# Optimization experiments

Measured on AMD Instinct MI355X. Metric: run time of the kernel, lower is better.

Reference implementation:

```python
import jax, jax.numpy as jnp
import numpy as np

INPUT_DIM = 512
HIDDEN_DIM = 512
B, N = 8, 2048


def setup_inputs() -> dict:
    key = jax.random.key(0)
    ks = jax.random.split(key, 9)
    s_in = 1.0 / np.sqrt(INPUT_DIM)
    s_h = 1.0 / np.sqrt(HIDDEN_DIM)
    return {
        "X": jax.random.normal(ks[0], (B, N, INPUT_DIM), dtype=jnp.float32),
        "Wq": jax.random.uniform(ks[1], (INPUT_DIM, HIDDEN_DIM), minval=-s_in, maxval=s_in),
        "bq": jnp.zeros((HIDDEN_DIM,), jnp.float32),
        "Wk": jax.random.uniform(ks[2], (INPUT_DIM, HIDDEN_DIM), minval=-s_in, maxval=s_in),
        "bk": jnp.zeros((HIDDEN_DIM,), jnp.float32),
        "Wv": jax.random.uniform(ks[3], (INPUT_DIM, HIDDEN_DIM), minval=-s_in, maxval=s_in),
        "bv": jnp.zeros((HIDDEN_DIM,), jnp.float32),
        "Wo": jax.random.uniform(ks[4], (HIDDEN_DIM, INPUT_DIM), minval=-s_h, maxval=s_h),
        "bo": jnp.zeros((INPUT_DIM,), jnp.float32),
        "ln_gamma": jnp.ones((INPUT_DIM,), jnp.float32),
        "ln_beta": jnp.zeros((INPUT_DIM,), jnp.float32),
    }


def reference(X, Wq, bq, Wk, bk, Wv, bv, Wo, bo, ln_gamma, ln_beta):
    q = X @ Wq + bq                      # [B,N,H]
    k = X @ Wk + bk
    v = X @ Wv + bv
    scores = jnp.einsum('bnh,bmh->bnm', q, k) / jnp.sqrt(jnp.float32(HIDDEN_DIM))
    attn = jax.nn.softmax(scores, axis=-1)      # [B,N,N]
    ctx = jnp.einsum('bnm,bmh->bnh', attn, v)   # [B,N,H]
    out = ctx @ Wo + bo + X                      # residual
    mu = jnp.mean(out, axis=-1, keepdims=True)
    var = jnp.var(out, axis=-1, keepdims=True)
    normed = (out - mu) / jnp.sqrt(var + 1e-5)
    return normed * ln_gamma + ln_beta
```

## Files before the change

### kernel.cpp

```cpp
#include <hip/hip_runtime.h>
#include <cstdint>
#include <cstddef>


typedef __bf16 bf16x8 __attribute__((ext_vector_type(8)));
typedef float  f32x4  __attribute__((ext_vector_type(4)));

__device__ __forceinline__ uint16_t f2bf(float f) {
  union { float f; uint32_t u; } v; v.f = f;
  uint32_t r = v.u + 0x7FFFu + ((v.u >> 16) & 1u);
  return (uint16_t)(r >> 16);
}

__device__ __forceinline__ void gld16(const uint16_t* g, uint16_t* l) {
  __builtin_amdgcn_global_load_lds(
      (__attribute__((address_space(1))) void*)(g),
      (__attribute__((address_space(3))) void*)(l), 16, 0, 0);
}

template <int MODE, int BM, int BN, int WM, int WN>
__global__ __launch_bounds__(512, 4) void gemm_k(
    const uint16_t* __restrict__ A, const uint16_t* __restrict__ Bt,
    void* __restrict__ OutA, uint16_t* __restrict__ OutK,
    uint16_t* __restrict__ OutVT, float* __restrict__ rsum, int K, int lda,
    int ldb, const float* __restrict__ b0, const float* __restrict__ b1,
    const float* __restrict__ b2, const float* __restrict__ Xres, float scale) {
  constexpr int MT = (BM / WM) / 16;
  constexpr int NT = (BN / WN) / 16;
  constexpr int AI = BM / 128;
  constexpr int BI = BN / 128;
  constexpr int PW = AI + BI;
  __shared__ alignas(16) uint16_t As[3][BM * 32];
  __shared__ alignas(16) uint16_t Bs[3][BN * 32];

  const int tid = threadIdx.x;
  const int w = tid >> 6, lane = tid & 63;
  const int wm = w / WN, wn = w % WN;

  const int gx = gridDim.x, gy = gridDim.y;
  const int nwg = gx * gy * gridDim.z;
  const int hw = blockIdx.x + gx * (blockIdx.y + gy * blockIdx.z);
  const int lg = (hw & 7) * (nwg >> 3) + (hw >> 3);
  const int bx = lg % gx, byz = lg / gx;
  const int by = byz % gy, z = byz / gy;

  const int m0 = by * BM, n0 = bx * BN;

  const uint16_t* Ab = A;
  const uint16_t* Bb = Bt;
  if (MODE == 1) { Ab += (size_t)z * 2048 * 512;  Bb += (size_t)z * 2048 * 512; }
  if (MODE == 2) { Ab += (size_t)z * 2048 * 2048; Bb += (size_t)z * 512 * 2048; }

  const int kc = (((lane & 3) ^ ((lane >> 2) & 3) ^ (lane >> 4)) * 8);
  const int rbA = w * (BM / 8);
  const int rbB = w * (BN / 8);
  const uint16_t* gA = Ab + (size_t)(m0 + rbA + (lane >> 2)) * lda + kc;
  const uint16_t* gB = Bb + (size_t)(n0 + rbB + (lane >> 2)) * ldb + kc;

  f32x4 acc[MT][NT];
#pragma unroll
  for (int i = 0; i < MT; i++)
#pragma unroll
    for (int j = 0; j < NT; j++) acc[i][j] = (f32x4){0.f, 0.f, 0.f, 0.f};

  const int lr = lane & 15;
  const int swz = (((lane >> 4) ^ (lr & 3) ^ (lr >> 2)) * 8);
  const int iters = K >> 5;

  auto stage = [&](int t, int buf) {
    const int k0 = t * 32;
#pragma unroll
    for (int j = 0; j < AI; j++)
      gld16(gA + k0 + (size_t)(j * 16) * lda, &As[buf][(rbA + j * 16) * 32]);
#pragma unroll
    for (int j = 0; j < BI; j++)
      gld16(gB + k0 + (size_t)(j * 16) * ldb, &Bs[buf][(rbB + j * 16) * 32]);
  };

  auto compute = [&](int buf) {
    bf16x8 af[MT], bfr[NT];
#pragma unroll
    for (int t = 0; t < MT; t++)
      af[t] = *(const bf16x8*)&As[buf][(wm * (BM / WM) + t * 16 + lr) * 32 + swz];
#pragma unroll
    for (int t = 0; t < NT; t++)
      bfr[t] = *(const bf16x8*)&Bs[buf][(wn * (BN / WN) + t * 16 + lr) * 32 + swz];
#pragma unroll
    for (int nt = 0; nt < NT; nt++)
#pragma unroll
      for (int mt = 0; mt < MT; mt++)
        acc[mt][nt] = __builtin_amdgcn_mfma_f32_16x16x32_bf16(
            af[mt], bfr[nt], acc[mt][nt], 0, 0, 0);
  };

  stage(0, 0);
  stage(1, 1);
  int buf = 0;
  for (int i = 0; i < iters - 1; ++i) {
    asm volatile("s_waitcnt vmcnt(%0)" ::"i"(PW) : "memory");
    __builtin_amdgcn_s_barrier();
    if (i + 2 < iters) stage(i + 2, (buf + 2 >= 3) ? buf - 1 : buf + 2);
    compute(buf);
    buf = (buf == 2) ? 0 : buf + 1;
  }
  asm volatile("s_waitcnt vmcnt(0)" ::: "memory");
  __builtin_amdgcn_s_barrier();
  compute(buf);

  if (MODE == 1) {
    uint16_t* Sp = (uint16_t*)OutA + (size_t)z * 2048 * 2048;
#pragma unroll
    for (int mt = 0; mt < MT; mt++) {
      float rp[4] = {0.f, 0.f, 0.f, 0.f};
#pragma unroll
      for (int nt = 0; nt < NT; nt++) {
#pragma unroll
        for (int i = 0; i < 4; i++) {
          const int row = m0 + wm * (BM / WM) + mt * 16 + (lane >> 4) * 4 + i;
          const int col = n0 + wn * (BN / WN) + nt * 16 + lr;
          const float e = __expf(acc[mt][nt][i] * scale);
          Sp[(size_t)row * 2048 + col] = f2bf(e);
          rp[i] += e;
        }
      }
#pragma unroll
      for (int i = 0; i < 4; i++) {
        float p = rp[i];
        p += __shfl_xor(p, 1); p += __shfl_xor(p, 2);
        p += __shfl_xor(p, 4); p += __shfl_xor(p, 8);
        if (lr == 0) {
          const int row = m0 + wm * (BM / WM) + mt * 16 + (lane >> 4) * 4 + i;
          atomicAdd(&rsum[z * 2048 + row], p);
        }
      }
    }
  } else if (MODE == 2) {
#pragma unroll
    for (int mt = 0; mt < MT; mt++) {
#pragma unroll
      for (int i = 0; i < 4; i++) {
        const int row = m0 + wm * (BM / WM) + mt * 16 + (lane >> 4) * 4 + i;
        const float sc = 1.0f / rsum[z * 2048 + row];
#pragma unroll
        for (int nt = 0; nt < NT; nt++) {
          const int col = n0 + wn * (BN / WN) + nt * 16 + lr;
          ((uint16_t*)OutA)[((size_t)z * 2048 + row) * 512 + col] =
              f2bf(acc[mt][nt][i] * sc);
        }
      }
    }
  } else {
#pragma unroll
    for (int mt = 0; mt < MT; mt++) {
#pragma unroll
      for (int nt = 0; nt < NT; nt++) {
#pragma unroll
        for (int i = 0; i < 4; i++) {
          const int row = m0 + wm * (BM / WM) + mt * 16 + (lane >> 4) * 4 + i;
          const int col = n0 + wn * (BN / WN) + nt * 16 + lr;
          const float v = acc[mt][nt][i];
          if (MODE == 0) {
            const int which = col >> 9, c = col & 511;
            if (which == 0) {
              ((uint16_t*)OutA)[(size_t)row * 512 + c] = f2bf(v + b0[c]);
            } else if (which == 1) {
              OutK[(size_t)row * 512 + c] = f2bf(v + b1[c]);
            } else {
              OutVT[(size_t)(row >> 11) * (512 * 2048) + (size_t)c * 2048 +
                    (row & 2047)] = f2bf(v + b2[c]);
            }
          } else {
            const size_t idx = (size_t)row * 512 + col;
            ((float*)OutA)[idx] = v + b0[col] + Xres[idx];
          }
        }
      }
    }
  }
}

__global__ __launch_bounds__(256) void cvt_all_k(
    const float* __restrict__ X, uint16_t* __restrict__ Xb,
    const float* __restrict__ Wq, const float* __restrict__ Wk,
    const float* __restrict__ Wv, const float* __restrict__ Wo,
    uint16_t* __restrict__ Wt, float* __restrict__ rsum) {
  const int i = blockIdx.x * 256 + threadIdx.x;
  const float4 f = ((const float4*)X)[i];
  uint32_t lo = (uint32_t)f2bf(f.x) | ((uint32_t)f2bf(f.y) << 16);
  uint32_t hi = (uint32_t)f2bf(f.z) | ((uint32_t)f2bf(f.w) << 16);
  ((uint2*)Xb)[i] = make_uint2(lo, hi);
  if (i < 16384) rsum[i] = 0.f;
  if (i < 2048 * 512) {
    const int n = i >> 9, kk = i & 511;
    const int which = n >> 9, c = n & 511;
    const float* W =
        (which == 0) ? Wq : (which == 1) ? Wk : (which == 2) ? Wv : Wo;
    Wt[i] = f2bf(W[kk * 512 + c]);
  }
}

__global__ __launch_bounds__(256) void ln_k(float* __restrict__ O,
                                            const float* __restrict__ g,
                                            const float* __restrict__ b) {
  const int tid = threadIdx.x, w = tid >> 6, lane = tid & 63;
  float* p = O + ((size_t)blockIdx.x * 4 + w) * 512;
  float4 v0 = ((const float4*)p)[lane];
  float4 v1 = ((const float4*)p)[64 + lane];
  float s  = v0.x + v0.y + v0.z + v0.w + v1.x + v1.y + v1.z + v1.w;
  float sq = v0.x * v0.x + v0.y * v0.y + v0.z * v0.z + v0.w * v0.w +
             v1.x * v1.x + v1.y * v1.y + v1.z * v1.z + v1.w * v1.w;
#pragma unroll
  for (int off = 32; off >= 1; off >>= 1) {
    s += __shfl_xor(s, off);
    sq += __shfl_xor(sq, off);
  }
  const float mean = s * (1.f / 512.f);
  const float var = sq * (1.f / 512.f) - mean * mean;
  const float rstd = rsqrtf(var + 1e-5f);
  const float4 g0 = ((const float4*)g)[lane], g1 = ((const float4*)g)[64 + lane];
  const float4 b0 = ((const float4*)b)[lane], b1 = ((const float4*)b)[64 + lane];
  v0.x = (v0.x - mean) * rstd * g0.x + b0.x;
  v0.y = (v0.y - mean) * rstd * g0.y + b0.y;
  v0.z = (v0.z - mean) * rstd * g0.z + b0.z;
  v0.w = (v0.w - mean) * rstd * g0.w + b0.w;
  v1.x = (v1.x - mean) * rstd * g1.x + b1.x;
  v1.y = (v1.y - mean) * rstd * g1.y + b1.y;
  v1.z = (v1.z - mean) * rstd * g1.z + b1.z;
  v1.w = (v1.w - mean) * rstd * g1.w + b1.w;
  ((float4*)p)[lane] = v0;
  ((float4*)p)[64 + lane] = v1;
}

extern "C" void kernel_launch(void* const* d_in, const int* in_sizes, int n_in,
                              void* d_out, int out_size, void* d_ws,
                              size_t ws_size, hipStream_t stream) {
  const float* X     = (const float*)d_in[0];
  const float* Wq    = (const float*)d_in[1];
  const float* bq    = (const float*)d_in[2];
  const float* bk    = (const float*)d_in[4];
  const float* Wk    = (const float*)d_in[3];
  const float* Wv    = (const float*)d_in[5];
  const float* bv    = (const float*)d_in[6];
  const float* Wo    = (const float*)d_in[7];
  const float* bo    = (const float*)d_in[8];
  const float* gamma = (const float*)d_in[9];
  const float* beta  = (const float*)d_in[10];
  float* out = (float*)d_out;

  char* ws = (char*)d_ws;
  uint16_t* S    = (uint16_t*)(ws);
  uint16_t* Xb   = (uint16_t*)(ws);
  uint16_t* Wt   = (uint16_t*)(ws + 67108864);
  uint16_t* q    = (uint16_t*)(ws + 69206016);
  uint16_t* kb   = (uint16_t*)(ws + 85983232);
  uint16_t* vT   = (uint16_t*)(ws + 102760448);
  float*    rsum = (float*)(ws + 119537664);
  uint16_t* ctx  = q;

  cvt_all_k<<<dim3(8192), dim3(256), 0, stream>>>(X, Xb, Wq, Wk, Wv, Wo, Wt,
                                                  rsum);
  gemm_k<0, 256, 128, 4, 2><<<dim3(12, 64, 1), dim3(512), 0, stream>>>(
      Xb, Wt, (void*)q, kb, vT, nullptr, 512, 512, 512, bq, bk, bv, nullptr,
      1.f);
  gemm_k<1, 256, 128, 4, 2><<<dim3(16, 8, 8), dim3(512), 0, stream>>>(
      q, kb, (void*)S, nullptr, nullptr, rsum, 512, 512, 512, nullptr, nullptr,
      nullptr, nullptr, 0.044194173824159216f);
  gemm_k<2, 256, 128, 4, 2><<<dim3(4, 8, 8), dim3(512), 0, stream>>>(
      S, vT, (void*)ctx, nullptr, nullptr, rsum, 2048, 2048, 2048, nullptr,
      nullptr, nullptr, nullptr, 1.f);
  gemm_k<3, 256, 128, 4, 2><<<dim3(4, 64, 1), dim3(512), 0, stream>>>(
      ctx, Wt + 1536 * 512, (void*)out, nullptr, nullptr, nullptr, 512, 512,
      512, bo, nullptr, nullptr, X, 1.f);
  ln_k<<<dim3(4096), dim3(256), 0, stream>>>(out, gamma, beta);
}
```

Before: 317.6 us.

## Restructure GEMM main loop with 64-wide K tiles and interleaved staging phases

Doubles the K tile per stage from 32 to 64 with a new XOR swizzle. Each K tile is split into two half-phases that interleave global-to-LDS staging with MFMA bursts raised via s_setprio. Occupancy hint drops to 2 blocks per SM to fit the larger LDS buffers. The goal is fewer barriers per unit of work and better overlap of loads with matrix math, at the cost of geometry fixed by static_assert and reduced occupancy.

```diff
diff --git a/kernel.cpp b/kernel.cpp
--- a/kernel.cpp
+++ b/kernel.cpp
@@ -19,19 +19,21 @@
 }
 
 template <int MODE, int BM, int BN, int WM, int WN>
-__global__ __launch_bounds__(512, 4) void gemm_k(
+__global__ __launch_bounds__(512, 2) void gemm_k(
     const uint16_t* __restrict__ A, const uint16_t* __restrict__ Bt,
     void* __restrict__ OutA, uint16_t* __restrict__ OutK,
     uint16_t* __restrict__ OutVT, float* __restrict__ rsum, int K, int lda,
     int ldb, const float* __restrict__ b0, const float* __restrict__ b1,
     const float* __restrict__ b2, const float* __restrict__ Xres, float scale) {
-  constexpr int MT = (BM / WM) / 16;
-  constexpr int NT = (BN / WN) / 16;
-  constexpr int AI = BM / 128;
-  constexpr int BI = BN / 128;
-  constexpr int PW = AI + BI;
-  __shared__ alignas(16) uint16_t As[3][BM * 32];
-  __shared__ alignas(16) uint16_t Bs[3][BN * 32];
+  constexpr int WR = BM / WM;
+  constexpr int WC = BN / WN;
+  constexpr int MT = WR / 16;
+  constexpr int NT = WC / 16;
+  constexpr int SA = BM / 64;
+  constexpr int SB = BN / 64;
+  static_assert(WR == 64 && WC == 64 && SA == 4 && SB == 2, "geometry");
+  __shared__ alignas(16) uint16_t As[3][BM * 64];
+  __shared__ alignas(16) uint16_t Bs[3][BN * 64];
 
   const int tid = threadIdx.x;
   const int w = tid >> 6, lane = tid & 63;
@@ -51,11 +53,18 @@
   if (MODE == 1) { Ab += (size_t)z * 2048 * 512;  Bb += (size_t)z * 2048 * 512; }
   if (MODE == 2) { Ab += (size_t)z * 2048 * 2048; Bb += (size_t)z * 512 * 2048; }
 
-  const int kc = (((lane & 3) ^ ((lane >> 2) & 3) ^ (lane >> 4)) * 8);
-  const int rbA = w * (BM / 8);
-  const int rbB = w * (BN / 8);
-  const uint16_t* gA = Ab + (size_t)(m0 + rbA + (lane >> 2)) * lda + kc;
-  const uint16_t* gB = Bb + (size_t)(n0 + rbB + (lane >> 2)) * ldb + kc;
+  const int l3 = lane >> 3, l7 = lane & 7;
+  const int csw = (l7 ^ l3) * 8;
+  const uint16_t* gAb = Ab + (size_t)(m0 + w * 8 + l3) * lda + csw;
+  const uint16_t* gBb = Bb + (size_t)(n0 + w * 8 + l3) * ldb + csw;
+  const int ldsw = w * 512;
+
+  auto stageA = [&](int v, int bufb, int kg) {
+    gld16(gAb + (size_t)(v * 64) * lda + kg, &As[bufb][v * 4096 + ldsw]);
+  };
+  auto stageB = [&](int v, int bufb, int kg) {
+    gld16(gBb + (size_t)(v * 64) * ldb + kg, &Bs[bufb][v * 4096 + ldsw]);
+  };
 
   f32x4 acc[MT][NT];
 #pragma unroll
@@ -63,49 +72,65 @@
 #pragma unroll
     for (int j = 0; j < NT; j++) acc[i][j] = (f32x4){0.f, 0.f, 0.f, 0.f};
 
-  const int lr = lane & 15;
-  const int swz = (((lane >> 4) ^ (lr & 3) ^ (lr >> 2)) * 8);
-  const int iters = K >> 5;
-
-  auto stage = [&](int t, int buf) {
-    const int k0 = t * 32;
-#pragma unroll
-    for (int j = 0; j < AI; j++)
-      gld16(gA + k0 + (size_t)(j * 16) * lda, &As[buf][(rbA + j * 16) * 32]);
-#pragma unroll
-    for (int j = 0; j < BI; j++)
-      gld16(gB + k0 + (size_t)(j * 16) * ldb, &Bs[buf][(rbB + j * 16) * 32]);
-  };
-
-  auto compute = [&](int buf) {
-    bf16x8 af[MT], bfr[NT];
-#pragma unroll
-    for (int t = 0; t < MT; t++)
-      af[t] = *(const bf16x8*)&As[buf][(wm * (BM / WM) + t * 16 + lr) * 32 + swz];
-#pragma unroll
-    for (int t = 0; t < NT; t++)
-      bfr[t] = *(const bf16x8*)&Bs[buf][(wn * (BN / WN) + t * 16 + lr) * 32 + swz];
-#pragma unroll
-    for (int nt = 0; nt < NT; nt++)
-#pragma unroll
-      for (int mt = 0; mt < MT; mt++)
-        acc[mt][nt] = __builtin_amdgcn_mfma_f32_16x16x32_bf16(
-            af[mt], bfr[nt], acc[mt][nt], 0, 0, 0);
-  };
-
-  stage(0, 0);
-  stage(1, 1);
-  int buf = 0;
-  for (int i = 0; i < iters - 1; ++i) {
-    asm volatile("s_waitcnt vmcnt(%0)" ::"i"(PW) : "memory");
-    __builtin_amdgcn_s_barrier();
-    if (i + 2 < iters) stage(i + 2, (buf + 2 >= 3) ? buf - 1 : buf + 2);
-    compute(buf);
-    buf = (buf == 2) ? 0 : buf + 1;
-  }
-  asm volatile("s_waitcnt vmcnt(0)" ::: "memory");
+  const int lr = lane & 15, q4 = lane >> 4;
+  const int rc0 = ((q4) ^ l7) * 8;
+  const int rc1 = ((4 + q4) ^ l7) * 8;
+
+  const int NK = K >> 6;
+
+#pragma unroll
+  for (int u = 0; u < SA; u++) stageA(u, 0, 0);
+#pragma unroll
+  for (int u = 0; u < SB; u++) stageB(u, 0, 0);
+#pragma unroll
+  for (int u = 0; u < SA; u++) stageA(u, 1, 64);
+#pragma unroll
+  for (int u = 0; u < SB; u++) stageB(u, 1, 64);
+  asm volatile("s_waitcnt vmcnt(6)" ::: "memory");
   __builtin_amdgcn_s_barrier();
-  compute(buf);
+
+#define QPHASE(QM, S0, S1, S2, DRAIN)                                          \
+  {                                                                            \
+    bf16x8 af0[2], af1[2], bv0[4], bv1[4];                                     \
+    _Pragma("unroll") for (int t = 0; t < 2; t++) {                            \
+      const int ra = (wm * 64 + (QM) * 32 + t * 16 + lr) * 64;                 \
+      af0[t] = *(const bf16x8*)&As[cb][ra + rc0];                              \
+      af1[t] = *(const bf16x8*)&As[cb][ra + rc1];                              \
+    }                                                                          \
+    _Pragma("unroll") for (int t = 0; t < 4; t++) {                            \
+      const int rb = (wn * 64 + t * 16 + lr) * 64;                             \
+      bv0[t] = *(const bf16x8*)&Bs[cb][rb + rc0];                              \
+      bv1[t] = *(const bf16x8*)&Bs[cb][rb + rc1];                              \
+    }                                                                          \
+    if (st) { S0; S1; S2; }                                                    \
+    __builtin_amdgcn_s_barrier();                                              \
+    __builtin_amdgcn_s_setprio(1);                                             \
+    _Pragma("unroll") for (int nt = 0; nt < 4; nt++)                           \
+      _Pragma("unroll") for (int mt = 0; mt < 2; mt++)                         \
+        acc[(QM) * 2 + mt][nt] = __builtin_amdgcn_mfma_f32_16x16x32_bf16(      \
+            af0[mt], bv0[nt], acc[(QM) * 2 + mt][nt], 0, 0, 0);                \
+    _Pragma("unroll") for (int nt = 0; nt < 4; nt++)                           \
+      _Pragma("unroll") for (int mt = 0; mt < 2; mt++)                         \
+        acc[(QM) * 2 + mt][nt] = __builtin_amdgcn_mfma_f32_16x16x32_bf16(      \
+            af1[mt], bv1[nt], acc[(QM) * 2 + mt][nt], 0, 0, 0);                \
+    __builtin_amdgcn_s_setprio(0);                                             \
+    DRAIN;                                                                     \
+    __builtin_amdgcn_s_barrier();                                              \
+  }
+
+  for (int kt = 0; kt < NK; ++kt) {
+    const int cb = kt % 3;
+    const int sbuf = (kt + 2) % 3;
+    const bool st = (kt + 2) < NK;
+    const int kg = (kt + 2) << 6;
+    QPHASE(0, stageA(0, sbuf, kg), stageA(1, sbuf, kg), stageA(2, sbuf, kg), )
+    QPHASE(1, stageA(3, sbuf, kg), stageB(0, sbuf, kg), stageB(1, sbuf, kg),
+           if (kt + 1 < NK) {
+             if (st) { asm volatile("s_waitcnt vmcnt(6)" ::: "memory"); }
+             else    { asm volatile("s_waitcnt vmcnt(0)" ::: "memory"); }
+           })
+  }
+#undef QPHASE
 
   if (MODE == 1) {
     uint16_t* Sp = (uint16_t*)OutA + (size_t)z * 2048 * 2048;
@@ -116,8 +141,8 @@
       for (int nt = 0; nt < NT; nt++) {
 #pragma unroll
         for (int i = 0; i < 4; i++) {
-          const int row = m0 + wm * (BM / WM) + mt * 16 + (lane >> 4) * 4 + i;
-          const int col = n0 + wn * (BN / WN) + nt * 16 + lr;
+          const int row = m0 + wm * WR + mt * 16 + (lane >> 4) * 4 + i;
+          const int col = n0 + wn * WC + nt * 16 + lr;
           const float e = __expf(acc[mt][nt][i] * scale);
           Sp[(size_t)row * 2048 + col] = f2bf(e);
           rp[i] += e;
@@ -129,7 +154,7 @@
         p += __shfl_xor(p, 1); p += __shfl_xor(p, 2);
         p += __shfl_xor(p, 4); p += __shfl_xor(p, 8);
         if (lr == 0) {
-          const int row = m0 + wm * (BM / WM) + mt * 16 + (lane >> 4) * 4 + i;
+          const int row = m0 + wm * WR + mt * 16 + (lane >> 4) * 4 + i;
           atomicAdd(&rsum[z * 2048 + row], p);
         }
       }
@@ -139,11 +164,11 @@
     for (int mt = 0; mt < MT; mt++) {
 #pragma unroll
       for (int i = 0; i < 4; i++) {
-        const int row = m0 + wm * (BM / WM) + mt * 16 + (lane >> 4) * 4 + i;
+        const int row = m0 + wm * WR + mt * 16 + (lane >> 4) * 4 + i;
         const float sc = 1.0f / rsum[z * 2048 + row];
 #pragma unroll
         for (int nt = 0; nt < NT; nt++) {
-          const int col = n0 + wn * (BN / WN) + nt * 16 + lr;
+          const int col = n0 + wn * WC + nt * 16 + lr;
           ((uint16_t*)OutA)[((size_t)z * 2048 + row) * 512 + col] =
               f2bf(acc[mt][nt][i] * sc);
         }
@@ -156,8 +181,8 @@
       for (int nt = 0; nt < NT; nt++) {
 #pragma unroll
         for (int i = 0; i < 4; i++) {
-          const int row = m0 + wm * (BM / WM) + mt * 16 + (lane >> 4) * 4 + i;
-          const int col = n0 + wn * (BN / WN) + nt * 16 + lr;
+          const int row = m0 + wm * WR + mt * 16 + (lane >> 4) * 4 + i;
+          const int col = n0 + wn * WC + nt * 16 + lr;
           const float v = acc[mt][nt][i];
           if (MODE == 0) {
             const int which = col >> 9, c = col & 511;
@@ -237,8 +262,8 @@
   const float* X     = (const float*)d_in[0];
   const float* Wq    = (const float*)d_in[1];
   const float* bq    = (const float*)d_in[2];
+  const float* Wk    = (const float*)d_in[3];
   const float* bk    = (const float*)d_in[4];
-  const float* Wk    = (const float*)d_in[3];
   const float* Wv    = (const float*)d_in[5];
   const float* bv    = (const float*)d_in[6];
   const float* Wo    = (const float*)d_in[7];
```

Result: slower. 337.6 us (+6.3%).

## Fuse LayerNorm into output projection GEMM with full-row tiles

Applied to the files above, without the earlier changes.

Replaces the output-projection GEMM plus the separate LayerNorm kernel with a single GEMM variant. It uses 64x512 tiles, so each block owns whole rows and can add bias and residual, reduce sum and sum-of-squares across its 8 waves through shared memory, then write normalized output. This drops the extra launch and the fp32 read/write round trip of the output tensor. In exchange the block needs a large LDS footprint (B tile of 512 rows across 3 buffers), so occupancy is lower. The upper four waves also redundantly reload the A tile.

```diff
diff --git a/kernel.cpp b/kernel.cpp
--- a/kernel.cpp
+++ b/kernel.cpp
@@ -27,7 +27,8 @@
     const float* __restrict__ b2, const float* __restrict__ Xres, float scale) {
   constexpr int MT = (BM / WM) / 16;
   constexpr int NT = (BN / WN) / 16;
-  constexpr int AI = BM / 128;
+  static_assert(MT == 4 && NT == 4, "wave tile must be 64x64");
+  constexpr int AI = (BM >= 128) ? BM / 128 : 1;
   constexpr int BI = BN / 128;
   constexpr int PW = AI + BI;
   __shared__ alignas(16) uint16_t As[3][BM * 32];
@@ -52,7 +53,7 @@
   if (MODE == 2) { Ab += (size_t)z * 2048 * 2048; Bb += (size_t)z * 512 * 2048; }
 
   const int kc = (((lane & 3) ^ ((lane >> 2) & 3) ^ (lane >> 4)) * 8);
-  const int rbA = w * (BM / 8);
+  const int rbA = (BM >= 128) ? w * (BM / 8) : (w & 3) * 16;
   const int rbB = w * (BN / 8);
   const uint16_t* gA = Ab + (size_t)(m0 + rbA + (lane >> 2)) * lda + kc;
   const uint16_t* gB = Bb + (size_t)(n0 + rbB + (lane >> 2)) * ldb + kc;
@@ -63,7 +64,7 @@
 #pragma unroll
     for (int j = 0; j < NT; j++) acc[i][j] = (f32x4){0.f, 0.f, 0.f, 0.f};
 
-  const int lr = lane & 15;
+  const int lr = lane & 15, q4 = lane >> 4;
   const int swz = (((lane >> 4) ^ (lr & 3) ^ (lr >> 2)) * 8);
   const int iters = K >> 5;
 
@@ -116,7 +117,7 @@
       for (int nt = 0; nt < NT; nt++) {
 #pragma unroll
         for (int i = 0; i < 4; i++) {
-          const int row = m0 + wm * (BM / WM) + mt * 16 + (lane >> 4) * 4 + i;
+          const int row = m0 + wm * (BM / WM) + mt * 16 + q4 * 4 + i;
           const int col = n0 + wn * (BN / WN) + nt * 16 + lr;
           const float e = __expf(acc[mt][nt][i] * scale);
           Sp[(size_t)row * 2048 + col] = f2bf(e);
@@ -129,7 +130,7 @@
         p += __shfl_xor(p, 1); p += __shfl_xor(p, 2);
         p += __shfl_xor(p, 4); p += __shfl_xor(p, 8);
         if (lr == 0) {
-          const int row = m0 + wm * (BM / WM) + mt * 16 + (lane >> 4) * 4 + i;
+          const int row = m0 + wm * (BM / WM) + mt * 16 + q4 * 4 + i;
           atomicAdd(&rsum[z * 2048 + row], p);
         }
       }
@@ -139,7 +140,7 @@
     for (int mt = 0; mt < MT; mt++) {
 #pragma unroll
       for (int i = 0; i < 4; i++) {
-        const int row = m0 + wm * (BM / WM) + mt * 16 + (lane >> 4) * 4 + i;
+        const int row = m0 + wm * (BM / WM) + mt * 16 + q4 * 4 + i;
         const float sc = 1.0f / rsum[z * 2048 + row];
 #pragma unroll
         for (int nt = 0; nt < NT; nt++) {
@@ -149,6 +150,53 @@
         }
       }
     }
+  } else if (MODE == 4) {
+    __shared__ float redS[8][64];
+    __shared__ float redQ[8][64];
+    float* Op = (float*)OutA;
+    __syncthreads();
+#pragma unroll
+    for (int mt = 0; mt < MT; mt++) {
+#pragma unroll
+      for (int i = 0; i < 4; i++) {
+        const int rl = mt * 16 + q4 * 4 + i;
+        const int row = m0 + rl;
+        float ps = 0.f, pq = 0.f;
+#pragma unroll
+        for (int nt = 0; nt < NT; nt++) {
+          const int col = wn * 64 + nt * 16 + lr;
+          float v = acc[mt][nt][i] + b0[col] + Xres[(size_t)row * 512 + col];
+          acc[mt][nt][i] = v;
+          ps += v; pq += v * v;
+        }
+        ps += __shfl_xor(ps, 1); pq += __shfl_xor(pq, 1);
+        ps += __shfl_xor(ps, 2); pq += __shfl_xor(pq, 2);
+        ps += __shfl_xor(ps, 4); pq += __shfl_xor(pq, 4);
+        ps += __shfl_xor(ps, 8); pq += __shfl_xor(pq, 8);
+        if (lr == 0) { redS[w][rl] = ps; redQ[w][rl] = pq; }
+      }
+    }
+    __syncthreads();
+#pragma unroll
+    for (int mt = 0; mt < MT; mt++) {
+#pragma unroll
+      for (int i = 0; i < 4; i++) {
+        const int rl = mt * 16 + q4 * 4 + i;
+        const int row = m0 + rl;
+        float s8 = 0.f, q8 = 0.f;
+#pragma unroll
+        for (int ww = 0; ww < 8; ww++) { s8 += redS[ww][rl]; q8 += redQ[ww][rl]; }
+        const float mean = s8 * (1.f / 512.f);
+        const float var = q8 * (1.f / 512.f) - mean * mean;
+        const float rstd = rsqrtf(var + 1e-5f);
+#pragma unroll
+        for (int nt = 0; nt < NT; nt++) {
+          const int col = wn * 64 + nt * 16 + lr;
+          Op[(size_t)row * 512 + col] =
+              (acc[mt][nt][i] - mean) * rstd * b1[col] + b2[col];
+        }
+      }
+    }
   } else {
 #pragma unroll
     for (int mt = 0; mt < MT; mt++) {
@@ -156,22 +204,17 @@
       for (int nt = 0; nt < NT; nt++) {
 #pragma unroll
         for (int i = 0; i < 4; i++) {
-          const int row = m0 + wm * (BM / WM) + mt * 16 + (lane >> 4) * 4 + i;
+          const int row = m0 + wm * (BM / WM) + mt * 16 + q4 * 4 + i;
           const int col = n0 + wn * (BN / WN) + nt * 16 + lr;
           const float v = acc[mt][nt][i];
-          if (MODE == 0) {
-            const int which = col >> 9, c = col & 511;
-            if (which == 0) {
-              ((uint16_t*)OutA)[(size_t)row * 512 + c] = f2bf(v + b0[c]);
-            } else if (which == 1) {
-              OutK[(size_t)row * 512 + c] = f2bf(v + b1[c]);
-            } else {
-              OutVT[(size_t)(row >> 11) * (512 * 2048) + (size_t)c * 2048 +
-                    (row & 2047)] = f2bf(v + b2[c]);
-            }
+          const int which = col >> 9, c = col & 511;
+          if (which == 0) {
+            ((uint16_t*)OutA)[(size_t)row * 512 + c] = f2bf(v + b0[c]);
+          } else if (which == 1) {
+            OutK[(size_t)row * 512 + c] = f2bf(v + b1[c]);
           } else {
-            const size_t idx = (size_t)row * 512 + col;
-            ((float*)OutA)[idx] = v + b0[col] + Xres[idx];
+            OutVT[(size_t)(row >> 11) * (512 * 2048) + (size_t)c * 2048 +
+                  (row & 2047)] = f2bf(v + b2[c]);
           }
         }
       }
@@ -199,46 +242,14 @@
   }
 }
 
-__global__ __launch_bounds__(256) void ln_k(float* __restrict__ O,
-                                            const float* __restrict__ g,
-                                            const float* __restrict__ b) {
-  const int tid = threadIdx.x, w = tid >> 6, lane = tid & 63;
-  float* p = O + ((size_t)blockIdx.x * 4 + w) * 512;
-  float4 v0 = ((const float4*)p)[lane];
-  float4 v1 = ((const float4*)p)[64 + lane];
-  float s  = v0.x + v0.y + v0.z + v0.w + v1.x + v1.y + v1.z + v1.w;
-  float sq = v0.x * v0.x + v0.y * v0.y + v0.z * v0.z + v0.w * v0.w +
-             v1.x * v1.x + v1.y * v1.y + v1.z * v1.z + v1.w * v1.w;
-#pragma unroll
-  for (int off = 32; off >= 1; off >>= 1) {
-    s += __shfl_xor(s, off);
-    sq += __shfl_xor(sq, off);
-  }
-  const float mean = s * (1.f / 512.f);
-  const float var = sq * (1.f / 512.f) - mean * mean;
-  const float rstd = rsqrtf(var + 1e-5f);
-  const float4 g0 = ((const float4*)g)[lane], g1 = ((const float4*)g)[64 + lane];
-  const float4 b0 = ((const float4*)b)[lane], b1 = ((const float4*)b)[64 + lane];
-  v0.x = (v0.x - mean) * rstd * g0.x + b0.x;
-  v0.y = (v0.y - mean) * rstd * g0.y + b0.y;
-  v0.z = (v0.z - mean) * rstd * g0.z + b0.z;
-  v0.w = (v0.w - mean) * rstd * g0.w + b0.w;
-  v1.x = (v1.x - mean) * rstd * g1.x + b1.x;
-  v1.y = (v1.y - mean) * rstd * g1.y + b1.y;
-  v1.z = (v1.z - mean) * rstd * g1.z + b1.z;
-  v1.w = (v1.w - mean) * rstd * g1.w + b1.w;
-  ((float4*)p)[lane] = v0;
-  ((float4*)p)[64 + lane] = v1;
-}
-
 extern "C" void kernel_launch(void* const* d_in, const int* in_sizes, int n_in,
                               void* d_out, int out_size, void* d_ws,
                               size_t ws_size, hipStream_t stream) {
   const float* X     = (const float*)d_in[0];
   const float* Wq    = (const float*)d_in[1];
   const float* bq    = (const float*)d_in[2];
+  const float* Wk    = (const float*)d_in[3];
   const float* bk    = (const float*)d_in[4];
-  const float* Wk    = (const float*)d_in[3];
   const float* Wv    = (const float*)d_in[5];
   const float* bv    = (const float*)d_in[6];
   const float* Wo    = (const float*)d_in[7];
@@ -268,8 +279,7 @@
   gemm_k<2, 256, 128, 4, 2><<<dim3(4, 8, 8), dim3(512), 0, stream>>>(
       S, vT, (void*)ctx, nullptr, nullptr, rsum, 2048, 2048, 2048, nullptr,
       nullptr, nullptr, nullptr, 1.f);
-  gemm_k<3, 256, 128, 4, 2><<<dim3(4, 64, 1), dim3(512), 0, stream>>>(
+  gemm_k<4, 64, 512, 1, 8><<<dim3(1, 256, 1), dim3(512), 0, stream>>>(
       ctx, Wt + 1536 * 512, (void*)out, nullptr, nullptr, nullptr, 512, 512,
-      512, bo, nullptr, nullptr, X, 1.f);
-  ln_k<<<dim3(4096), dim3(256), 0, stream>>>(out, gamma, beta);
-}
+      512, bo, gamma, beta, X, 1.f);
+}
```

Result: no change. 316.8 us (-0.3%).
